# Performance work log

Hardware: AMD Instinct MI355X
Metric: run time of the kernel (lower is better)

The kernel has to match this reference:

```python
import jax, jax.numpy as jnp
import numpy as np

EPS = 1e-5
NEG_SLOPE = 0.2
N_NODES, N_EDGES, F_IN, HID, HEADS, N_GRAPHS, N_CLS = 20000, 320000, 128, 256, 4, 128, 10
D_HEAD = HID // HEADS

def _bn(x, g, b):
    # BatchNorm1d, training-mode batch statistics (biased var), weight=g, bias=b
    m = x.mean(0)
    v = x.var(0)
    return (x - m) * jax.lax.rsqrt(v + EPS) * g + b

def _gat(x, src, dst, n, W, a_src, a_dst, bias):
    # PyG GATConv: linear -> per-head attention logits -> dst-segment softmax -> scatter-add
    xp = (x @ W).reshape(n, HEADS, D_HEAD)                 # [N,H,D]
    als = jnp.einsum('nhd,hd->nh', xp, a_src)              # alpha_src per node
    ald = jnp.einsum('nhd,hd->nh', xp, a_dst)
    e = jax.nn.leaky_relu(als[src] + ald[dst], NEG_SLOPE)  # [E,H]
    m = jax.ops.segment_max(e, dst, num_segments=n)
    p = jnp.exp(e - m[dst])
    s = jax.ops.segment_sum(p, dst, num_segments=n)
    alpha = p / s[dst]                                      # neighbor softmax
    msg = xp[src] * alpha[:, :, None]                       # [E,H,D]
    out = jax.ops.segment_sum(msg, dst, num_segments=n)
    return out.reshape(n, HID) + bias

def setup_inputs() -> dict:
    key = jax.random.key(0)
    ks = jax.random.split(key, 16)
    sc = lambda *sh: 1.0 / np.sqrt(sh[-2] if len(sh) >= 2 else sh[-1])
    inp = {
        'x': jax.random.normal(ks[0], (N_NODES, F_IN), jnp.float32),
        'edge_index': jax.random.randint(ks[1], (2, N_EDGES), 0, N_NODES, jnp.int32),
        'batch': jnp.sort(jax.random.randint(ks[2], (N_NODES,), 0, N_GRAPHS, jnp.int32)),
        'bn_feat_g': jnp.ones((F_IN,)), 'bn_feat_b': jnp.full((F_IN,), 1e-4),
        'W_feat': jax.random.normal(ks[3], (F_IN, HID)) * (1.0/np.sqrt(F_IN)),
        'b_feat': jnp.zeros((HID,)),
        'bns_g': jnp.ones((3, HID)), 'bns_b': jnp.full((3, HID), 1e-4),
        'Wg': jax.random.normal(ks[4], (3, HID, HID)) * (1.0/np.sqrt(HID)),
        'att_src': jax.random.normal(ks[5], (3, HEADS, D_HEAD)) * 0.1,
        'att_dst': jax.random.normal(ks[6], (3, HEADS, D_HEAD)) * 0.1,
        'gat_b': jnp.zeros((3, HID)),
        'bn_fc_g': jnp.ones((HID,)), 'bn_fc_b': jnp.full((HID,), 1e-4),
        'W_fc': jax.random.normal(ks[7], (HID, HID)) * (1.0/np.sqrt(HID)),
        'b_fc': jnp.zeros((HID,)),
        'bn_h_g': jnp.ones((HID,)), 'bn_h_b': jnp.full((HID,), 1e-4),
        'W_cls': jax.random.normal(ks[8], (HID, N_CLS)) * (1.0/np.sqrt(HID)),
        'b_cls': jnp.zeros((N_CLS,)),
    }
    return inp

def reference(x, edge_index, batch, bn_feat_g, bn_feat_b, W_feat, b_feat,
              bns_g, bns_b, Wg, att_src, att_dst, gat_b,
              bn_fc_g, bn_fc_b, W_fc, b_fc, bn_h_g, bn_h_b, W_cls, b_cls):
    n = x.shape[0]
    loops = jnp.arange(n, dtype=edge_index.dtype)
    src = jnp.concatenate([edge_index[0], loops])  # add self-loops (PyG GATConv)
    dst = jnp.concatenate([edge_index[1], loops])
    h = _bn(x, bn_feat_g, bn_feat_b)
    h = jax.nn.relu(h @ W_feat + b_feat)           # GCNConv(gfn=True): pure linear
    for i in range(3):
        h = _bn(h, bns_g[i], bns_b[i])
        h = jax.nn.relu(_gat(h, src, dst, n, Wg[i], att_src[i], att_dst[i], gat_b[i]))
    g = jax.ops.segment_sum(h, batch, num_segments=N_GRAPHS)  # global_add_pool
    g = _bn(g, bn_fc_g, bn_fc_b)
    g = jax.nn.relu(g @ W_fc + b_fc)
    g = _bn(g, bn_h_g, bn_h_b)
    logits = g @ W_cls + b_cls
    return jax.nn.log_softmax(logits, axis=-1)
```

## Files before the change

kernel.cpp:

```cpp
#include <hip/hip_runtime.h>

constexpr int NN   = 20000;
constexpr int NE   = 320000;
constexpr int NTOT = NE + NN;
constexpr int FIN  = 128;
constexpr int HID  = 256;
constexpr int NG   = 128;
constexpr int NCLS = 10;

typedef __bf16 bf16x8 __attribute__((ext_vector_type(8)));
typedef float  f32x4  __attribute__((ext_vector_type(4)));

__device__ __forceinline__ unsigned short f2b(float f) {
  unsigned u = __float_as_uint(f);
  unsigned r = (u + 0x7fffu + ((u >> 16) & 1u)) >> 16;
  return (unsigned short)r;
}
__device__ __forceinline__ float b2f(unsigned short h) {
  return __uint_as_float((unsigned)h << 16);
}

__global__ __launch_bounds__(256) void colstats_f32_kernel(const float* __restrict__ X, int M,
                                    float* __restrict__ ps, float* __restrict__ pss,
                                    unsigned short* __restrict__ xb) {
  __shared__ float sm[8][FIN], sq[8][FIN];
  int t = threadIdx.x;
  int g = t & 31, rs = t >> 5;
  int c0 = g * 4;
  float s0 = 0.f, s1 = 0.f, s2 = 0.f, s3 = 0.f;
  float q0 = 0.f, q1 = 0.f, q2 = 0.f, q3 = 0.f;
  for (int r = blockIdx.x + 256 * rs; r < M; r += 2048) {
    float4 v = *reinterpret_cast<const float4*>(X + (size_t)r * FIN + c0);
    ushort4 p;
    p.x = f2b(v.x); p.y = f2b(v.y); p.z = f2b(v.z); p.w = f2b(v.w);
    *reinterpret_cast<ushort4*>(xb + (size_t)r * FIN + c0) = p;
    s0 += v.x; q0 += v.x * v.x;
    s1 += v.y; q1 += v.y * v.y;
    s2 += v.z; q2 += v.z * v.z;
    s3 += v.w; q3 += v.w * v.w;
  }
  sm[rs][c0 + 0] = s0; sm[rs][c0 + 1] = s1; sm[rs][c0 + 2] = s2; sm[rs][c0 + 3] = s3;
  sq[rs][c0 + 0] = q0; sq[rs][c0 + 1] = q1; sq[rs][c0 + 2] = q2; sq[rs][c0 + 3] = q3;
  __syncthreads();
  if (t < FIN) {
    float S = 0.f, Q = 0.f;
#pragma unroll
    for (int k = 0; k < 8; ++k) { S += sm[k][t]; Q += sq[k][t]; }
    ps[blockIdx.x * 256 + t] = S;
    pss[blockIdx.x * 256 + t] = Q;
  }
}

__global__ __launch_bounds__(256) void colstats_bf16_kernel(const unsigned short* __restrict__ X, int M,
                                     float* __restrict__ ps, float* __restrict__ pss) {
  __shared__ float sm[8][HID], sq[8][HID];
  int t = threadIdx.x;
  int g = t & 31, rs = t >> 5;
  int c0 = g * 8;
  float s0 = 0.f, s1 = 0.f, s2 = 0.f, s3 = 0.f, s4 = 0.f, s5 = 0.f, s6 = 0.f, s7 = 0.f;
  float q0 = 0.f, q1 = 0.f, q2 = 0.f, q3 = 0.f, q4 = 0.f, q5 = 0.f, q6 = 0.f, q7 = 0.f;
  for (int r = blockIdx.x + 256 * rs; r < M; r += 2048) {
    uint4 w = *reinterpret_cast<const uint4*>(X + (size_t)r * HID + c0);
    float v;
    v = b2f((unsigned short)(w.x & 0xffff)); s0 += v; q0 += v * v;
    v = b2f((unsigned short)(w.x >> 16));    s1 += v; q1 += v * v;
    v = b2f((unsigned short)(w.y & 0xffff)); s2 += v; q2 += v * v;
    v = b2f((unsigned short)(w.y >> 16));    s3 += v; q3 += v * v;
    v = b2f((unsigned short)(w.z & 0xffff)); s4 += v; q4 += v * v;
    v = b2f((unsigned short)(w.z >> 16));    s5 += v; q5 += v * v;
    v = b2f((unsigned short)(w.w & 0xffff)); s6 += v; q6 += v * v;
    v = b2f((unsigned short)(w.w >> 16));    s7 += v; q7 += v * v;
  }
  sm[rs][c0 + 0] = s0; sm[rs][c0 + 1] = s1; sm[rs][c0 + 2] = s2; sm[rs][c0 + 3] = s3;
  sm[rs][c0 + 4] = s4; sm[rs][c0 + 5] = s5; sm[rs][c0 + 6] = s6; sm[rs][c0 + 7] = s7;
  sq[rs][c0 + 0] = q0; sq[rs][c0 + 1] = q1; sq[rs][c0 + 2] = q2; sq[rs][c0 + 3] = q3;
  sq[rs][c0 + 4] = q4; sq[rs][c0 + 5] = q5; sq[rs][c0 + 6] = q6; sq[rs][c0 + 7] = q7;
  __syncthreads();
  {
    float S = 0.f, Q = 0.f;
#pragma unroll
    for (int k = 0; k < 8; ++k) { S += sm[k][t]; Q += sq[k][t]; }
    ps[blockIdx.x * 256 + t] = S;
    pss[blockIdx.x * 256 + t] = Q;
  }
}

__global__ void finalize_stats(const float* __restrict__ ps, const float* __restrict__ pss,
                               const float* __restrict__ g, const float* __restrict__ b,
                               float invM, float* __restrict__ scale, float* __restrict__ shift) {
  int c = blockIdx.x, t = threadIdx.x;
  float s = 0.f, ss = 0.f;
#pragma unroll
  for (int k = 0; k < 4; ++k) {
    s  += ps[(t + k * 64) * 256 + c];
    ss += pss[(t + k * 64) * 256 + c];
  }
#pragma unroll
  for (int off = 32; off; off >>= 1) {
    s += __shfl_xor(s, off);
    ss += __shfl_xor(ss, off);
  }
  if (t == 0) {
    float m = s * invM;
    float v = ss * invM - m * m;
    float sc = g[c] * rsqrtf(v + 1e-5f);
    scale[c] = sc;
    shift[c] = b[c] - m * sc;
  }
}

__global__ __launch_bounds__(256) void wfold_kernel(const float* __restrict__ W,
    const float* __restrict__ scale, const float* __restrict__ shift,
    const float* __restrict__ bias_in, unsigned short* __restrict__ Wt,
    float* __restrict__ bias2, int K) {
  int n = blockIdx.x;
  int t = threadIdx.x;
  float part = 0.f;
  if (t < K) {
    float wv = W[(size_t)t * 256 + n];
    Wt[(size_t)n * K + t] = f2b(scale[t] * wv);
    part = shift[t] * wv;
  }
  __shared__ float red[256];
  red[t] = part;
  __syncthreads();
  if (t < 128) red[t] += red[t + 128];
  __syncthreads();
  if (t < 64) {
    float s = red[t] + red[t + 64];
#pragma unroll
    for (int off = 32; off; off >>= 1) s += __shfl_xor(s, off);
    if (t == 0) bias2[n] = (bias_in ? bias_in[n] : 0.f) + s;
  }
}

__global__ __launch_bounds__(256) void gemm_bf16_kernel(
    const unsigned short* __restrict__ Ab, const unsigned short* __restrict__ Wt,
    const float* __restrict__ bias2, unsigned short* __restrict__ Cb,
    int M, int K, int do_relu,
    float* __restrict__ als, float* __restrict__ ald,
    const float* __restrict__ asrc, const float* __restrict__ adst) {
  __shared__ unsigned short Am[128][40];
  __shared__ unsigned short Bn[128][40];
  int tid = threadIdx.x;
  int lane = tid & 63, wid = tid >> 6;
  int wm = wid >> 1, wn = wid & 1;
  int bm = blockIdx.x * 128, bn = blockIdx.y * 128;
  int lrow = lane & 15, lkh = (lane >> 4) * 8;
  int sr = tid >> 2;
  int ssg = tid & 3;

  f32x4 acc[4][4] = {};

  for (int k0 = 0; k0 < K; k0 += 32) {
    {
      int ra = min(bm + sr, M - 1);
      uint4 v0 = *reinterpret_cast<const uint4*>(Ab + (size_t)ra * K + k0 + ssg * 8);
      *reinterpret_cast<uint4*>(&Am[sr][ssg * 8]) = v0;
      int rb = min(bm + sr + 64, M - 1);
      uint4 v1 = *reinterpret_cast<const uint4*>(Ab + (size_t)rb * K + k0 + ssg * 8);
      *reinterpret_cast<uint4*>(&Am[sr + 64][ssg * 8]) = v1;
      uint4 w0 = *reinterpret_cast<const uint4*>(Wt + (size_t)(bn + sr) * K + k0 + ssg * 8);
      *reinterpret_cast<uint4*>(&Bn[sr][ssg * 8]) = w0;
      uint4 w1 = *reinterpret_cast<const uint4*>(Wt + (size_t)(bn + sr + 64) * K + k0 + ssg * 8);
      *reinterpret_cast<uint4*>(&Bn[sr + 64][ssg * 8]) = w1;
    }
    __syncthreads();
    bf16x8 af[4], bfr[4];
#pragma unroll
    for (int i = 0; i < 4; ++i)
      af[i] = *reinterpret_cast<const bf16x8*>(&Am[wm * 64 + i * 16 + lrow][lkh]);
#pragma unroll
    for (int j = 0; j < 4; ++j)
      bfr[j] = *reinterpret_cast<const bf16x8*>(&Bn[wn * 64 + j * 16 + lrow][lkh]);
#pragma unroll
    for (int i = 0; i < 4; ++i)
#pragma unroll
      for (int j = 0; j < 4; ++j)
        acc[i][j] = __builtin_amdgcn_mfma_f32_16x16x32_bf16(af[i], bfr[j], acc[i][j], 0, 0, 0);
    __syncthreads();
  }

  int r4 = (lane >> 4) * 4;
  bool att = (als != nullptr);
  int head = (bn >> 6) + wn;
  float bv[4], asv[4], adv[4];
#pragma unroll
  for (int j = 0; j < 4; ++j) {
    int colv = bn + wn * 64 + j * 16 + lrow;
    bv[j] = bias2[colv];
    if (att) { asv[j] = asrc[colv]; adv[j] = adst[colv]; }
  }
#pragma unroll
  for (int i = 0; i < 4; ++i) {
#pragma unroll
    for (int r = 0; r < 4; ++r) {
      int row = bm + wm * 64 + i * 16 + r4 + r;
      float ps = 0.f, pd = 0.f;
#pragma unroll
      for (int j = 0; j < 4; ++j) {
        int colv = bn + wn * 64 + j * 16 + lrow;
        float v = acc[i][j][r] + bv[j];
        if (do_relu) v = fmaxf(v, 0.f);
        if (row < M) Cb[(size_t)row * HID + colv] = f2b(v);
        if (att) { ps += v * asv[j]; pd += v * adv[j]; }
      }
      if (att) {
#pragma unroll
        for (int off = 1; off < 16; off <<= 1) {
          ps += __shfl_xor(ps, off);
          pd += __shfl_xor(pd, off);
        }
        if (lrow == 0 && row < M) {
          als[row * 4 + head] = ps;
          ald[row * 4 + head] = pd;
        }
      }
    }
  }
}

__device__ __forceinline__ void edge_sd(const int* __restrict__ ei, int e, int& s, int& d) {
  if (e < NE) { s = ei[e]; d = ei[NE + e]; }
  else        { s = e - NE; d = s; }
}

__global__ void hist_kernel(const int* __restrict__ ei, int* __restrict__ deg) {
  int e = blockIdx.x * blockDim.x + threadIdx.x;
  if (e >= NTOT) return;
  int s, d; edge_sd(ei, e, s, d);
  atomicAdd(&deg[d], 1);
}

__global__ __launch_bounds__(1024) void scan_kernel(const int* __restrict__ deg,
                                                    int* __restrict__ rp,
                                                    int* __restrict__ cursor) {
  __shared__ int part[1024];
  int t = threadIdx.x;
  const int C = (NN + 1023) / 1024;
  int base = t * C;
  int s = 0;
  for (int i = 0; i < C; ++i) {
    int idx = base + i;
    if (idx < NN) s += deg[idx];
  }
  part[t] = s;
  __syncthreads();
  for (int off = 1; off < 1024; off <<= 1) {
    int u = (t >= off) ? part[t - off] : 0;
    __syncthreads();
    part[t] += u;
    __syncthreads();
  }
  int run = part[t] - s;
  for (int i = 0; i < C; ++i) {
    int idx = base + i;
    if (idx < NN) {
      rp[idx] = run;
      cursor[idx] = run;
      run += deg[idx];
    }
  }
  if (t == 1023) rp[NN] = part[1023];
}

__global__ void scatter_kernel(const int* __restrict__ ei, int* __restrict__ cursor,
                               int* __restrict__ col) {
  int e = blockIdx.x * blockDim.x + threadIdx.x;
  if (e >= NTOT) return;
  int s, d; edge_sd(ei, e, s, d);
  int pos = atomicAdd(&cursor[d], 1);
  col[pos] = s;
}

__global__ __launch_bounds__(256) void gat_agg_kernel(
    const int* __restrict__ rp, const int* __restrict__ col,
    const float* __restrict__ als, const float* __restrict__ ald,
    const unsigned short* __restrict__ xp, const float* __restrict__ bias,
    unsigned short* __restrict__ out) {
  int wv = threadIdx.x >> 6, lane = threadIdx.x & 63;
  int n = blockIdx.x * 4 + wv;
  if (n >= NN) return;
  int beg = rp[n], deg = rp[n + 1] - beg;
  int hh = lane & 3;
  int jof = lane >> 2;
  float aldh = ald[n * 4 + hh];
  const int MAXR = 4;
  int   sN[MAXR];
  float lN[MAXR];
  int nr = (deg + 15) >> 4;
  int nrc = nr < MAXR ? nr : MAXR;
  float m = -1e30f;
#pragma unroll
  for (int r = 0; r < MAXR; ++r) {
    int s = 0; float l = -1e30f;
    if (r < nrc) {
      int j = r * 16 + jof;
      if (j < deg) {
        s = col[beg + j];
        l = als[s * 4 + hh] + aldh;
        l = l > 0.f ? l : 0.2f * l;
        m = fmaxf(m, l);
      }
    }
    sN[r] = s; lN[r] = l;
  }
  for (int r = MAXR; r < nr; ++r) {
    int j = r * 16 + jof;
    if (j < deg) {
      int s = col[beg + j];
      float l = als[s * 4 + hh] + aldh;
      l = l > 0.f ? l : 0.2f * l;
      m = fmaxf(m, l);
    }
  }
#pragma unroll
  for (int off = 4; off < 64; off <<= 1) m = fmaxf(m, __shfl_xor(m, off));
  int c0 = lane * 4;
  int hme = lane >> 4;
  float ss = 0.f;
  float a0 = 0.f, a1 = 0.f, a2 = 0.f, a3 = 0.f;
#pragma unroll
  for (int r = 0; r < MAXR; ++r) {
    if (r < nrc) {
      int sreg = sN[r];
      float cf = __expf(lN[r] - m);
      ss += cf;
      int cnt = min(16, deg - r * 16);
      if (cnt == 16) {
#pragma unroll
        for (int jj = 0; jj < 16; ++jj) {
          int s = __shfl(sreg, jj << 2);
          float c = __shfl(cf, (jj << 2) | hme);
          uint2 w = *reinterpret_cast<const uint2*>(xp + (size_t)s * HID + c0);
          a0 += c * b2f((unsigned short)(w.x & 0xffff));
          a1 += c * b2f((unsigned short)(w.x >> 16));
          a2 += c * b2f((unsigned short)(w.y & 0xffff));
          a3 += c * b2f((unsigned short)(w.y >> 16));
        }
      } else {
        for (int jj = 0; jj < cnt; ++jj) {
          int s = __shfl(sreg, jj << 2);
          float c = __shfl(cf, (jj << 2) | hme);
          uint2 w = *reinterpret_cast<const uint2*>(xp + (size_t)s * HID + c0);
          a0 += c * b2f((unsigned short)(w.x & 0xffff));
          a1 += c * b2f((unsigned short)(w.x >> 16));
          a2 += c * b2f((unsigned short)(w.y & 0xffff));
          a3 += c * b2f((unsigned short)(w.y >> 16));
        }
      }
    }
  }
  for (int r = MAXR; r < nr; ++r) {
    int j = r * 16 + jof;
    int sreg = 0;
    float cf = 0.f;
    if (j < deg) {
      sreg = col[beg + j];
      float l = als[sreg * 4 + hh] + aldh;
      l = l > 0.f ? l : 0.2f * l;
      cf = __expf(l - m);
      ss += cf;
    }
    int cnt = min(16, deg - r * 16);
    for (int jj = 0; jj < cnt; ++jj) {
      int s = __shfl(sreg, jj << 2);
      float c = __shfl(cf, (jj << 2) | hme);
      uint2 w = *reinterpret_cast<const uint2*>(xp + (size_t)s * HID + c0);
      a0 += c * b2f((unsigned short)(w.x & 0xffff));
      a1 += c * b2f((unsigned short)(w.x >> 16));
      a2 += c * b2f((unsigned short)(w.y & 0xffff));
      a3 += c * b2f((unsigned short)(w.y >> 16));
    }
  }
#pragma unroll
  for (int off = 4; off < 64; off <<= 1) ss += __shfl_xor(ss, off);
  float inv = 1.0f / __shfl(ss, hme);
  float4 bvv = *reinterpret_cast<const float4*>(bias + c0);
  ushort4 o;
  o.x = f2b(fmaxf(a0 * inv + bvv.x, 0.f));
  o.y = f2b(fmaxf(a1 * inv + bvv.y, 0.f));
  o.z = f2b(fmaxf(a2 * inv + bvv.z, 0.f));
  o.w = f2b(fmaxf(a3 * inv + bvv.w, 0.f));
  *reinterpret_cast<ushort4*>(out + (size_t)n * HID + c0) = o;
}

__global__ void pool_kernel(const unsigned short* __restrict__ h, const int* __restrict__ batch,
                            float* __restrict__ g) {
  const int ROWS = (NN + 255) / 256;
  int r0 = blockIdx.x * ROWS;
  int r1 = min(r0 + ROWS, NN);
  if (r0 >= r1) return;
  int t = threadIdx.x;
  int cg = t & 63, rs = t >> 6;
  int c0 = cg * 4;
  float a0 = 0.f, a1 = 0.f, a2 = 0.f, a3 = 0.f;
  int cur = -1;
  for (int r = r0 + rs; r < r1; r += 4) {
    int b = batch[r];
    if (b != cur) {
      if (cur >= 0) {
        atomicAdd(&g[(size_t)cur * HID + c0 + 0], a0);
        atomicAdd(&g[(size_t)cur * HID + c0 + 1], a1);
        atomicAdd(&g[(size_t)cur * HID + c0 + 2], a2);
        atomicAdd(&g[(size_t)cur * HID + c0 + 3], a3);
        a0 = a1 = a2 = a3 = 0.f;
      }
      cur = b;
    }
    uint2 w = *reinterpret_cast<const uint2*>(h + (size_t)r * HID + c0);
    a0 += b2f((unsigned short)(w.x & 0xffff));
    a1 += b2f((unsigned short)(w.x >> 16));
    a2 += b2f((unsigned short)(w.y & 0xffff));
    a3 += b2f((unsigned short)(w.y >> 16));
  }
  if (cur >= 0) {
    atomicAdd(&g[(size_t)cur * HID + c0 + 0], a0);
    atomicAdd(&g[(size_t)cur * HID + c0 + 1], a1);
    atomicAdd(&g[(size_t)cur * HID + c0 + 2], a2);
    atomicAdd(&g[(size_t)cur * HID + c0 + 3], a3);
  }
}

__global__ void fc_bn_kernel(const float* __restrict__ gin, const float* __restrict__ gamma,
                             const float* __restrict__ beta, const float* __restrict__ W,
                             const float* __restrict__ b, float* __restrict__ gout) {
  __shared__ float row[HID];
  int g = blockIdx.x, t = threadIdx.x;
  float s = 0.f, ss = 0.f;
  for (int r = 0; r < NG; ++r) {
    float v = gin[r * HID + t];
    s += v; ss += v * v;
  }
  float mn = s / NG, var = ss / NG - mn * mn;
  float sc = gamma[t] * rsqrtf(var + 1e-5f);
  float sh = beta[t] - mn * sc;
  row[t] = gin[g * HID + t] * sc + sh;
  __syncthreads();
  float acc = b[t];
  for (int k = 0; k < HID; ++k) acc += row[k] * W[k * HID + t];
  gout[g * HID + t] = fmaxf(acc, 0.f);
}

__global__ void cls_bn_kernel(const float* __restrict__ gin, const float* __restrict__ gamma,
                              const float* __restrict__ beta, const float* __restrict__ W,
                              const float* __restrict__ b, float* __restrict__ out) {
  __shared__ float row[HID];
  __shared__ float logits[NCLS];
  int g = blockIdx.x, t = threadIdx.x;
  float s = 0.f, ss = 0.f;
  for (int r = 0; r < NG; ++r) {
    float v = gin[r * HID + t];
    s += v; ss += v * v;
  }
  float mn = s / NG, var = ss / NG - mn * mn;
  float sc = gamma[t] * rsqrtf(var + 1e-5f);
  float sh = beta[t] - mn * sc;
  row[t] = gin[g * HID + t] * sc + sh;
  __syncthreads();
  if (t < NCLS) {
    float a = b[t];
    for (int k = 0; k < HID; ++k) a += row[k] * W[k * NCLS + t];
    logits[t] = a;
  }
  __syncthreads();
  if (t == 0) {
    float mxv = -1e30f;
    for (int i = 0; i < NCLS; ++i) mxv = fmaxf(mxv, logits[i]);
    float se = 0.f;
    for (int i = 0; i < NCLS; ++i) se += expf(logits[i] - mxv);
    float lse = mxv + logf(se);
    for (int i = 0; i < NCLS; ++i) out[g * NCLS + i] = logits[i] - lse;
  }
}

extern "C" void kernel_launch(void* const* d_in, const int* in_sizes, int n_in,
                              void* d_out, int out_size, void* d_ws, size_t ws_size,
                              hipStream_t stream) {
  const float* x        = (const float*)d_in[0];
  const int*   ei       = (const int*)d_in[1];
  const int*   batch    = (const int*)d_in[2];
  const float* bn_feat_g = (const float*)d_in[3];
  const float* bn_feat_b = (const float*)d_in[4];
  const float* W_feat   = (const float*)d_in[5];
  const float* b_feat   = (const float*)d_in[6];
  const float* bns_g    = (const float*)d_in[7];
  const float* bns_b    = (const float*)d_in[8];
  const float* Wg       = (const float*)d_in[9];
  const float* att_src  = (const float*)d_in[10];
  const float* att_dst  = (const float*)d_in[11];
  const float* gat_b    = (const float*)d_in[12];
  const float* bn_fc_g  = (const float*)d_in[13];
  const float* bn_fc_b  = (const float*)d_in[14];
  const float* W_fc     = (const float*)d_in[15];
  const float* b_fc     = (const float*)d_in[16];
  const float* bn_h_g   = (const float*)d_in[17];
  const float* bn_h_b   = (const float*)d_in[18];
  const float* W_cls    = (const float*)d_in[19];
  const float* b_cls    = (const float*)d_in[20];

  char* ws = (char*)d_ws;
  size_t off = 0;
  auto alloc = [&](size_t bytes) -> void* {
    void* p = ws + off;
    off += (bytes + 255) & ~(size_t)255;
    return p;
  };
  float* psum   = (float*)alloc(256 * 256 * 4);
  float* psumsq = (float*)alloc(256 * 256 * 4);
  float* scale  = (float*)alloc(HID * 4);
  float* shift  = (float*)alloc(HID * 4);
  float* bias2  = (float*)alloc(HID * 4);
  float* als    = (float*)alloc((size_t)NN * 4 * 4);
  float* ald    = (float*)alloc((size_t)NN * 4 * 4);
  int*   deg    = (int*)alloc((size_t)NN * 4);
  int*   cursor = (int*)alloc((size_t)NN * 4);
  int*   rp     = (int*)alloc((size_t)(NN + 1) * 4);
  int*   col    = (int*)alloc((size_t)NTOT * 4);
  unsigned short* xb  = (unsigned short*)alloc((size_t)NN * FIN * 2);
  unsigned short* Wft = (unsigned short*)alloc((size_t)HID * FIN * 2);
  unsigned short* Wgt = (unsigned short*)alloc((size_t)HID * HID * 2);
  unsigned short* bufA = (unsigned short*)alloc((size_t)NN * HID * 2);
  unsigned short* xp   = (unsigned short*)alloc((size_t)NN * HID * 2);
  float* g0     = (float*)alloc((size_t)NG * HID * 4);
  float* g1     = (float*)alloc((size_t)NG * HID * 4);
  (void)ws_size; (void)n_in; (void)in_sizes; (void)out_size;

  const int ETHREADS = 256;
  const int EGRID = (NTOT + ETHREADS - 1) / ETHREADS;

  hipMemsetAsync(deg, 0, (size_t)NN * 4, stream);
  hist_kernel<<<EGRID, ETHREADS, 0, stream>>>(ei, deg);
  scan_kernel<<<1, 1024, 0, stream>>>(deg, rp, cursor);
  scatter_kernel<<<EGRID, ETHREADS, 0, stream>>>(ei, cursor, col);

  colstats_f32_kernel<<<256, 256, 0, stream>>>(x, NN, psum, psumsq, xb);
  finalize_stats<<<FIN, 64, 0, stream>>>(psum, psumsq, bn_feat_g, bn_feat_b,
                                         1.0f / NN, scale, shift);
  wfold_kernel<<<HID, 256, 0, stream>>>(W_feat, scale, shift, b_feat, Wft, bias2, FIN);
  gemm_bf16_kernel<<<dim3((NN + 127) / 128, 2), 256, 0, stream>>>(
      xb, Wft, bias2, bufA, NN, FIN, 1, nullptr, nullptr, nullptr, nullptr);

  for (int i = 0; i < 3; ++i) {
    colstats_bf16_kernel<<<256, 256, 0, stream>>>(bufA, NN, psum, psumsq);
    finalize_stats<<<HID, 64, 0, stream>>>(psum, psumsq, bns_g + i * HID, bns_b + i * HID,
                                           1.0f / NN, scale, shift);
    wfold_kernel<<<HID, 256, 0, stream>>>(Wg + (size_t)i * HID * HID, scale, shift,
                                          nullptr, Wgt, bias2, HID);
    gemm_bf16_kernel<<<dim3((NN + 127) / 128, 2), 256, 0, stream>>>(
        bufA, Wgt, bias2, xp, NN, HID, 0, als, ald,
        att_src + i * HID, att_dst + i * HID);
    gat_agg_kernel<<<(NN + 3) / 4, 256, 0, stream>>>(rp, col, als, ald, xp,
                                                     gat_b + i * HID, bufA);
  }

  hipMemsetAsync(g0, 0, (size_t)NG * HID * 4, stream);
  pool_kernel<<<256, HID, 0, stream>>>(bufA, batch, g0);
  fc_bn_kernel<<<NG, HID, 0, stream>>>(g0, bn_fc_g, bn_fc_b, W_fc, b_fc, g1);
  cls_bn_kernel<<<NG, HID, 0, stream>>>(g1, bn_h_g, bn_h_b, W_cls, b_cls, (float*)d_out);
}
```

Measured before the change: 322.2 us.

## Fuse BN stats finalize into weight fold and first GEMM epilogue

Removes the separate finalize_stats kernel: each wfold block now reduces the per-block partial sums itself and computes the BN scale and shift inline. The first GEMM's epilogue accumulates per-column sum and sum-of-squares of its output, which replaces one colstats_bf16 pass over the 20000x256 activation. The remaining colstats calls move to after each aggregation. The trade is that every wfold block redundantly rereads all partial sums, which adds L2 traffic, and the first-layer stats are taken on fp32 values before bf16 rounding.

After: 529.0 us. 1.64x slower.

```diff
diff --git a/kernel.cpp b/kernel.cpp
--- a/kernel.cpp
+++ b/kernel.cpp
@@ -85,41 +85,27 @@
   }
 }
 
-__global__ void finalize_stats(const float* __restrict__ ps, const float* __restrict__ pss,
-                               const float* __restrict__ g, const float* __restrict__ b,
-                               float invM, float* __restrict__ scale, float* __restrict__ shift) {
-  int c = blockIdx.x, t = threadIdx.x;
-  float s = 0.f, ss = 0.f;
-#pragma unroll
-  for (int k = 0; k < 4; ++k) {
-    s  += ps[(t + k * 64) * 256 + c];
-    ss += pss[(t + k * 64) * 256 + c];
-  }
-#pragma unroll
-  for (int off = 32; off; off >>= 1) {
-    s += __shfl_xor(s, off);
-    ss += __shfl_xor(ss, off);
-  }
-  if (t == 0) {
-    float m = s * invM;
-    float v = ss * invM - m * m;
-    float sc = g[c] * rsqrtf(v + 1e-5f);
-    scale[c] = sc;
-    shift[c] = b[c] - m * sc;
-  }
-}
-
 __global__ __launch_bounds__(256) void wfold_kernel(const float* __restrict__ W,
-    const float* __restrict__ scale, const float* __restrict__ shift,
-    const float* __restrict__ bias_in, unsigned short* __restrict__ Wt,
-    float* __restrict__ bias2, int K) {
+    const float* __restrict__ ps, const float* __restrict__ pss,
+    const float* __restrict__ g, const float* __restrict__ b,
+    const float* __restrict__ bias_in, float invM,
+    unsigned short* __restrict__ Wt, float* __restrict__ bias2, int K, int P) {
   int n = blockIdx.x;
   int t = threadIdx.x;
   float part = 0.f;
   if (t < K) {
+    float s = 0.f, sq = 0.f;
+    for (int j = 0; j < P; ++j) {
+      s  += ps[j * 256 + t];
+      sq += pss[j * 256 + t];
+    }
+    float m = s * invM;
+    float var = sq * invM - m * m;
+    float sc = g[t] * rsqrtf(var + 1e-5f);
+    float sh = b[t] - m * sc;
     float wv = W[(size_t)t * 256 + n];
-    Wt[(size_t)n * K + t] = f2b(scale[t] * wv);
-    part = shift[t] * wv;
+    Wt[(size_t)n * K + t] = f2b(sc * wv);
+    part = sh * wv;
   }
   __shared__ float red[256];
   red[t] = part;
@@ -139,9 +125,11 @@
     const float* __restrict__ bias2, unsigned short* __restrict__ Cb,
     int M, int K, int do_relu,
     float* __restrict__ als, float* __restrict__ ald,
-    const float* __restrict__ asrc, const float* __restrict__ adst) {
+    const float* __restrict__ asrc, const float* __restrict__ adst,
+    float* __restrict__ cps, float* __restrict__ cpss) {
   __shared__ unsigned short Am[128][40];
   __shared__ unsigned short Bn[128][40];
+  __shared__ float csum[2][128], cqsum[2][128];
   int tid = threadIdx.x;
   int lane = tid & 63, wid = tid >> 6;
   int wm = wid >> 1, wn = wid & 1;
@@ -183,8 +171,10 @@
 
   int r4 = (lane >> 4) * 4;
   bool att = (als != nullptr);
+  bool stats = (cps != nullptr);
   int head = (bn >> 6) + wn;
   float bv[4], asv[4], adv[4];
+  float cs[4] = {}, cq[4] = {};
 #pragma unroll
   for (int j = 0; j < 4; ++j) {
     int colv = bn + wn * 64 + j * 16 + lrow;
@@ -196,26 +186,52 @@
 #pragma unroll
     for (int r = 0; r < 4; ++r) {
       int row = bm + wm * 64 + i * 16 + r4 + r;
-      float ps = 0.f, pd = 0.f;
+      float pvs = 0.f, pvd = 0.f;
 #pragma unroll
       for (int j = 0; j < 4; ++j) {
         int colv = bn + wn * 64 + j * 16 + lrow;
         float v = acc[i][j][r] + bv[j];
         if (do_relu) v = fmaxf(v, 0.f);
-        if (row < M) Cb[(size_t)row * HID + colv] = f2b(v);
-        if (att) { ps += v * asv[j]; pd += v * adv[j]; }
+        if (row < M) {
+          Cb[(size_t)row * HID + colv] = f2b(v);
+          if (stats) { cs[j] += v; cq[j] += v * v; }
+        }
+        if (att) { pvs += v * asv[j]; pvd += v * adv[j]; }
       }
       if (att) {
 #pragma unroll
         for (int off = 1; off < 16; off <<= 1) {
-          ps += __shfl_xor(ps, off);
-          pd += __shfl_xor(pd, off);
+          pvs += __shfl_xor(pvs, off);
+          pvd += __shfl_xor(pvd, off);
         }
         if (lrow == 0 && row < M) {
-          als[row * 4 + head] = ps;
-          ald[row * 4 + head] = pd;
+          als[row * 4 + head] = pvs;
+          ald[row * 4 + head] = pvd;
         }
       }
+    }
+  }
+  if (stats) {
+#pragma unroll
+    for (int j = 0; j < 4; ++j) {
+#pragma unroll
+      for (int off = 16; off < 64; off <<= 1) {
+        cs[j] += __shfl_xor(cs[j], off);
+        cq[j] += __shfl_xor(cq[j], off);
+      }
+    }
+    if ((lane >> 4) == 0) {
+#pragma unroll
+      for (int j = 0; j < 4; ++j) {
+        int ci = wn * 64 + j * 16 + lrow;
+        csum[wm][ci] = cs[j];
+        cqsum[wm][ci] = cq[j];
+      }
+    }
+    __syncthreads();
+    if (tid < 128) {
+      cps[(size_t)blockIdx.x * 256 + bn + tid]  = csum[0][tid] + csum[1][tid];
+      cpss[(size_t)blockIdx.x * 256 + bn + tid] = cqsum[0][tid] + cqsum[1][tid];
     }
   }
 }
@@ -508,8 +524,6 @@
   };
   float* psum   = (float*)alloc(256 * 256 * 4);
   float* psumsq = (float*)alloc(256 * 256 * 4);
-  float* scale  = (float*)alloc(HID * 4);
-  float* shift  = (float*)alloc(HID * 4);
   float* bias2  = (float*)alloc(HID * 4);
   float* als    = (float*)alloc((size_t)NN * 4 * 4);
   float* ald    = (float*)alloc((size_t)NN * 4 * 4);
@@ -528,6 +542,7 @@
 
   const int ETHREADS = 256;
   const int EGRID = (NTOT + ETHREADS - 1) / ETHREADS;
+  const int GX = (NN + 127) / 128;
 
   hipMemsetAsync(deg, 0, (size_t)NN * 4, stream);
   hist_kernel<<<EGRID, ETHREADS, 0, stream>>>(ei, deg);
@@ -535,23 +550,24 @@
   scatter_kernel<<<EGRID, ETHREADS, 0, stream>>>(ei, cursor, col);
 
   colstats_f32_kernel<<<256, 256, 0, stream>>>(x, NN, psum, psumsq, xb);
-  finalize_stats<<<FIN, 64, 0, stream>>>(psum, psumsq, bn_feat_g, bn_feat_b,
-                                         1.0f / NN, scale, shift);
-  wfold_kernel<<<HID, 256, 0, stream>>>(W_feat, scale, shift, b_feat, Wft, bias2, FIN);
-  gemm_bf16_kernel<<<dim3((NN + 127) / 128, 2), 256, 0, stream>>>(
-      xb, Wft, bias2, bufA, NN, FIN, 1, nullptr, nullptr, nullptr, nullptr);
+  wfold_kernel<<<HID, 256, 0, stream>>>(W_feat, psum, psumsq, bn_feat_g, bn_feat_b,
+                                        b_feat, 1.0f / NN, Wft, bias2, FIN, 256);
+  gemm_bf16_kernel<<<dim3(GX, 2), 256, 0, stream>>>(
+      xb, Wft, bias2, bufA, NN, FIN, 1, nullptr, nullptr, nullptr, nullptr,
+      psum, psumsq);
 
   for (int i = 0; i < 3; ++i) {
-    colstats_bf16_kernel<<<256, 256, 0, stream>>>(bufA, NN, psum, psumsq);
-    finalize_stats<<<HID, 64, 0, stream>>>(psum, psumsq, bns_g + i * HID, bns_b + i * HID,
-                                           1.0f / NN, scale, shift);
-    wfold_kernel<<<HID, 256, 0, stream>>>(Wg + (size_t)i * HID * HID, scale, shift,
-                                          nullptr, Wgt, bias2, HID);
-    gemm_bf16_kernel<<<dim3((NN + 127) / 128, 2), 256, 0, stream>>>(
+    int P = (i == 0) ? GX : 256;
+    wfold_kernel<<<HID, 256, 0, stream>>>(Wg + (size_t)i * HID * HID, psum, psumsq,
+                                          bns_g + i * HID, bns_b + i * HID,
+                                          nullptr, 1.0f / NN, Wgt, bias2, HID, P);
+    gemm_bf16_kernel<<<dim3(GX, 2), 256, 0, stream>>>(
         bufA, Wgt, bias2, xp, NN, HID, 0, als, ald,
-        att_src + i * HID, att_dst + i * HID);
+        att_src + i * HID, att_dst + i * HID, nullptr, nullptr);
     gat_agg_kernel<<<(NN + 3) / 4, 256, 0, stream>>>(rp, col, als, ald, xp,
                                                      gat_b + i * HID, bufA);
+    if (i < 2)
+      colstats_bf16_kernel<<<256, 256, 0, stream>>>(bufA, NN, psum, psumsq);
   }
 
   hipMemsetAsync(g0, 0, (size_t)NG * HID * 4, stream);
```
